# Kernel optimization log

Hardware: AMD Instinct MI355X
Metric: run time of the kernel (lower is better)

The kernel has to match this reference:

```python
import jax, jax.numpy as jnp
import numpy as np

N_ITERS = 200   # fixed PDHG iterations (stands in for SCS max_iters)
POWER_ITERS = 30


def setup_inputs() -> dict:
    key = jax.random.key(0)
    k1, k2 = jax.random.split(key)
    B, n_hos, n_types, n_structs = 512, 16, 16, 4096
    m = n_hos * n_types
    # bids (capacities) are strictly positive counts
    X = jax.random.uniform(k1, (B, n_hos, n_types), jnp.float32, minval=1.0, maxval=10.0)
    # sparse 0/1 cycle-incidence matrix (each column = one feasible exchange structure)
    S = (jax.random.uniform(k2, (m, n_structs)) < 0.03).astype(jnp.float32)
    return {"X": X, "S": S, "batch_size": B}


def _solve_lp_batch(S, b, n_iters=N_ITERS):
    """Batched LP:  max 1^T x  s.t.  x >= 0,  S x <= b,  via Chambolle-Pock PDHG.

    S: [m, n] shared constraint matrix; b: [B, m] per-sample rhs.
    Returns x: [B, n] (the allocation that CvxpyLayer/SCS would return).
    """
    m, n = S.shape
    B = b.shape[0]
    w = jnp.ones((B, n), b.dtype)

    # spectral norm of S via power iteration -> step sizes
    v = jnp.ones((n,), S.dtype)

    def pw(v, _):
        v = S.T @ (S @ v)
        return v / jnp.linalg.norm(v), None

    v, _ = jax.lax.scan(pw, v, None, length=POWER_ITERS)
    L = jnp.sqrt(jnp.vdot(v, S.T @ (S @ v)))  # ~ ||S||_2
    tau = 0.9 / L
    sigma = 0.9 / L

    x0 = jnp.zeros((B, n), b.dtype)
    y0 = jnp.zeros((B, m), b.dtype)  # dual for Sx <= b

    def step(carry, _):
        x, y = carry
        # primal: gradient ascent on w^T x - y^T S x, projected to x >= 0
        x_new = jnp.maximum(x + tau * (w - y @ S), 0.0)        # [B,n]
        # dual: ascent on constraint residual with extrapolated primal, y >= 0
        y_new = jnp.maximum(y + sigma * ((2.0 * x_new - x) @ S.T - b), 0.0)  # [B,m]
        return (x_new, y_new), None

    (x, _), _ = jax.lax.scan(step, (x0, y0), None, length=n_iters)
    return x


def reference(X, S, batch_size):
    m, _ = S.shape
    b = X.reshape(batch_size, m)  # B = X.view(batch, n_hos*n_types)
    return _solve_lp_batch(S, b)  # [batch, n_structures]
```

## Files before the change

kernel.cpp:

```cpp
#include <hip/hip_runtime.h>

#define M 256
#define N 4096
#define NIT 200
#define PIT 30

#define YDUMMY (256*8)
#define ZDUMMY (4096*8)

__global__ void k_colcnt(const float* __restrict__ S, int* __restrict__ col_cnt){
  int j = blockIdx.x*256 + threadIdx.x;
  int c = 0;
  for (int i = 0; i < M; ++i) c += (S[i*N + j] != 0.0f) ? 1 : 0;
  col_cnt[j] = c;
}

__global__ void k_rowcnt(const float* __restrict__ S, int* __restrict__ row_cnt){
  int wid = blockIdx.x*(blockDim.x>>6) + (threadIdx.x>>6);
  int l = threadIdx.x & 63;
  if (wid >= M) return;
  int cnt = 0;
  for (int jc = 0; jc < N/64; ++jc){
    float v = S[wid*N + jc*64 + l];
    unsigned long long mask = __ballot(v != 0.0f);
    cnt += __popcll(mask);
  }
  if (l == 0) row_cnt[wid] = cnt;
}

__global__ void k_sortcol(const int* __restrict__ col_cnt,
                          int* __restrict__ col_perm, int* __restrict__ col_rank){
  __shared__ int cs[N];
  int t0 = threadIdx.x;
  for (int t = 0; t < N/256; ++t) cs[t0 + 256*t] = col_cnt[t0 + 256*t];
  __syncthreads();
  int j = blockIdx.x*256 + t0;
  int cj = cs[j];
  int rank = 0;
  #pragma unroll 4
  for (int jj = 0; jj < N; ++jj){
    int c = cs[jj];
    rank += ((c < cj) || (c == cj && jj < j)) ? 1 : 0;
  }
  col_perm[rank] = j;
  col_rank[j] = rank;
}

__global__ void k_sortrow(const int* __restrict__ row_cnt,
                          int* __restrict__ row_perm, int* __restrict__ row_rank){
  int i = threadIdx.x;
  int ci = row_cnt[i];
  int rank = 0;
  for (int ii = 0; ii < M; ++ii){
    int c = row_cnt[ii];
    rank += ((c < ci) || (c == ci && ii < i)) ? 1 : 0;
  }
  row_perm[rank] = i;
  row_rank[i] = rank;
}

__global__ void k_trips(const int* __restrict__ col_cnt, const int* __restrict__ col_perm,
                        const int* __restrict__ row_cnt, const int* __restrict__ row_perm,
                        int* __restrict__ pT4, int* __restrict__ pB4,
                        int* __restrict__ dT4, int* __restrict__ dB4){
  int tid = threadIdx.x;
  if (tid < 64){
    int k = tid >> 4, w = tid & 15;
    int mx = 0;
    for (int l = 0; l < 64; ++l){
      int s = 64*w + l + 1024*k;
      int c = col_cnt[col_perm[s]];
      mx = max(mx, c);
    }
    pT4[tid] = min((mx + 3) >> 2, 16);
  } else if (tid < 80){
    int w = tid - 64;
    int mx = 0;
    for (int l = 0; l < 64; ++l){
      int t = w*64 + l;
      int r = t >> 2, q = t & 3;
      int len = row_cnt[row_perm[r]];
      int qs = (len*q) >> 2, qe = (len*(q+1)) >> 2;
      mx = max(mx, qe - qs);
    }
    dT4[w] = min((mx + 3) >> 2, 80);
  }
  __syncthreads();
  if (tid == 0){
    int acc = 0;
    for (int i = 0; i < 64; ++i){ pB4[i] = acc; acc += pT4[i]; }
    acc = 0;
    for (int i = 0; i < 16; ++i){ dB4[i] = acc; acc += dT4[i]; }
  }
}

__global__ void k_fillp(const float* __restrict__ S, const int* __restrict__ col_rank,
                        const int* __restrict__ pT4, const int* __restrict__ pB4,
                        unsigned short* __restrict__ pstream){
  int j = blockIdx.x*256 + threadIdx.x;
  int sr = col_rank[j];
  int k = sr >> 10, rem = sr & 1023, w = rem >> 6, l = rem & 63;
  int kw = k*16 + w;
  int base = pB4[kw];
  int cap = pT4[kw]*4;
  int T = l & 15;
  int t = 0;
  for (int cc = 0; cc < 16 && t < cap; ++cc){
    int c = (T + cc) & 15;
    for (int i16 = 0; i16 < 16 && t < cap; ++i16){
      int i = i16*16 + c;
      if (S[i*N + j] != 0.0f){
        pstream[((base + (t>>2))*64 + l)*4 + (t&3)] = (unsigned short)(i*8);
        ++t;
      }
    }
  }
  for (; t < cap; ++t)
    pstream[((base + (t>>2))*64 + l)*4 + (t&3)] = (unsigned short)YDUMMY;
}

__global__ void k_filld(const float* __restrict__ S,
                        const int* __restrict__ row_cnt, const int* __restrict__ row_perm,
                        const int* __restrict__ dT4, const int* __restrict__ dB4,
                        unsigned short* __restrict__ dstream){
  int rr = blockIdx.x;
  int lf = threadIdx.x;
  int i  = row_perm[rr];
  int len = row_cnt[i];
  int c0 = rr & 15;
  int wc = rr >> 4;
  int base = dB4[wc];
  int cap  = dT4[wc]*4;
  int qs1 = (len*1) >> 2, qs2 = (len*2) >> 2, qs3 = (len*3) >> 2;
  int lc0 = (rr & 15) << 2;

  int pos = 0;
  for (int cc = 0; cc < 16; ++cc){
    int c = (c0 + cc) & 15;
    for (int mc = 0; mc < 4; ++mc){
      int m = mc*64 + lf;
      int j = c + 16*m;
      float v = S[i*N + j];
      unsigned long long mask = __ballot(v != 0.0f);
      if (v != 0.0f){
        int rank = pos + __popcll(mask & ((1ull << lf) - 1ull));
        int q = (rank >= qs1) + (rank >= qs2) + (rank >= qs3);
        int qs = (q==0) ? 0 : ((q==1) ? qs1 : ((q==2) ? qs2 : qs3));
        int t = rank - qs;
        if (t < cap)
          dstream[((base + (t>>2))*64 + (lc0 + q))*4 + (t&3)] = (unsigned short)(j*8);
      }
      pos += __popcll(mask);
    }
  }
  if (lf < 4){
    int q = lf;
    int qs = (q==0) ? 0 : ((q==1) ? qs1 : ((q==2) ? qs2 : qs3));
    int qe = (q==3) ? len : ((q==0) ? qs1 : ((q==1) ? qs2 : qs3));
    int qlen = qe - qs; if (qlen > cap) qlen = cap;
    for (int t = qlen; t < cap; ++t)
      dstream[((base + (t>>2))*64 + (lc0 + q))*4 + (t&3)] = (unsigned short)ZDUMMY;
  }
}

__global__ __launch_bounds__(1024) void k_power(
    const ushort4* __restrict__ pstream, const ushort4* __restrict__ dstream,
    const int* __restrict__ col_perm, const int* __restrict__ row_perm,
    const int* __restrict__ pT4, const int* __restrict__ pB4,
    const int* __restrict__ dT4, const int* __restrict__ dB4,
    float* __restrict__ tauw)
{
  __shared__ float2 v_s[N+8];
  __shared__ float2 u_s[M+8];
  __shared__ float2 red2[1024];
  const int tid = threadIdx.x, w = tid >> 6, l = tid & 63;

  int cj[4], pb[4], pt[4];
  float tl[4];
  #pragma unroll
  for (int k = 0; k < 4; ++k){
    int kw = k*16 + w;
    pb[k] = pB4[kw]; pt[k] = pT4[kw];
    cj[k] = col_perm[tid + 1024*k];
    v_s[cj[k]] = make_float2(1.0f, 0.0f);
    tl[k] = 0.0f;
  }
  const int r = tid >> 2, q = tid & 3;
  const int rid = row_perm[r];
  const int db = dB4[w], dt = dT4[w];
  if (tid < 8){ v_s[N+tid] = make_float2(0,0); u_s[M+tid] = make_float2(0,0); }
  __syncthreads();

  const char* vb = (const char*)v_s;
  const char* ub = (const char*)u_s;

  for (int it = 0; it < PIT; ++it){
    float a = 0.0f;
    for (int c = 0; c < dt; ++c){
      ushort4 ix = dstream[(db + c)*64 + l];
      a += ((const float2*)(vb + ix.x))->x + ((const float2*)(vb + ix.y))->x
         + ((const float2*)(vb + ix.z))->x + ((const float2*)(vb + ix.w))->x;
    }
    a += __shfl_xor(a, 1);
    a += __shfl_xor(a, 2);
    if (q == 0) u_s[rid] = make_float2(a, 0.0f);
    __syncthreads();
    #pragma unroll
    for (int k = 0; k < 4; ++k){
      float a2 = 0.0f;
      for (int c = 0; c < pt[k]; ++c){
        ushort4 ix = pstream[(pb[k] + c)*64 + l];
        a2 += ((const float2*)(ub + ix.x))->x + ((const float2*)(ub + ix.y))->x
            + ((const float2*)(ub + ix.z))->x + ((const float2*)(ub + ix.w))->x;
      }
      tl[k] = a2 * (1.0f/1024.0f);
      v_s[cj[k]] = make_float2(tl[k], 0.0f);
    }
    __syncthreads();
  }

  float pv = 0.0f;
  #pragma unroll
  for (int k = 0; k < 4; ++k) pv += tl[k]*tl[k];
  float a = 0.0f;
  for (int c = 0; c < dt; ++c){
    ushort4 ix = dstream[(db + c)*64 + l];
    a += ((const float2*)(vb + ix.x))->x + ((const float2*)(vb + ix.y))->x
       + ((const float2*)(vb + ix.z))->x + ((const float2*)(vb + ix.w))->x;
  }
  a += __shfl_xor(a, 1);
  a += __shfl_xor(a, 2);
  float fsq = (q == 0) ? a*a : 0.0f;
  red2[tid] = make_float2(pv, fsq);
  __syncthreads();
  for (int sd = 512; sd > 0; sd >>= 1){
    if (tid < sd){
      red2[tid].x += red2[tid+sd].x;
      red2[tid].y += red2[tid+sd].y;
    }
    __syncthreads();
  }
  if (tid == 0) tauw[0] = 0.9f * sqrtf(red2[0].x / red2[0].y);
}

__global__ __launch_bounds__(1024) void k_main(
    const float* __restrict__ X,
    const ushort4* __restrict__ pstream, const ushort4* __restrict__ dstream,
    const int* __restrict__ col_perm, const int* __restrict__ row_perm,
    const int* __restrict__ pT4, const int* __restrict__ pB4,
    const int* __restrict__ dT4, const int* __restrict__ dB4,
    const float* __restrict__ tauw, float* __restrict__ out)
{
  __shared__ float2 z_s[N+8];
  __shared__ float2 y_s[M+8];
  const int tid = threadIdx.x, w = tid >> 6, l = tid & 63;
  const int b0 = blockIdx.x * 2;
  const float tau = tauw[0];
  const float sigma = tau;

  int cj[4], pb[4], pt[4];
  float2 x[4];
  #pragma unroll
  for (int k = 0; k < 4; ++k){
    int kw = k*16 + w;
    pb[k] = pB4[kw]; pt[k] = pT4[kw];
    cj[k] = col_perm[tid + 1024*k];
    x[k] = make_float2(0.0f, 0.0f);
  }
  const int r = tid >> 2, q = tid & 3;
  const int rid = row_perm[r];
  const int db = dB4[w], dt = dT4[w];
  float2 bi = make_float2(0,0), yv = make_float2(0,0);
  if (q == 0){
    bi.x = X[b0*M + rid];
    bi.y = X[(b0+1)*M + rid];
    y_s[rid] = make_float2(0,0);
  }
  if (tid < 8){ y_s[M+tid] = make_float2(0,0); z_s[N+tid] = make_float2(0,0); }
  __syncthreads();

  const char* yb = (const char*)y_s;
  const char* zb = (const char*)z_s;

  for (int it = 0; it < NIT; ++it){
    const bool last = (it == NIT-1);
    #pragma unroll
    for (int k = 0; k < 4; ++k){
      float ax = 0.0f, ay = 0.0f;
      for (int c = 0; c < pt[k]; ++c){
        ushort4 ix = pstream[(pb[k] + c)*64 + l];
        float2 a0 = *(const float2*)(yb + ix.x);
        float2 a1 = *(const float2*)(yb + ix.y);
        float2 a2 = *(const float2*)(yb + ix.z);
        float2 a3 = *(const float2*)(yb + ix.w);
        ax += (a0.x + a1.x) + (a2.x + a3.x);
        ay += (a0.y + a1.y) + (a2.y + a3.y);
      }
      float2 xo = x[k];
      float xnx = fmaxf(xo.x + tau*(1.0f - ax), 0.0f);
      float xny = fmaxf(xo.y + tau*(1.0f - ay), 0.0f);
      if (!last) z_s[cj[k]] = make_float2(2.0f*xnx - xo.x, 2.0f*xny - xo.y);
      x[k] = make_float2(xnx, xny);
    }
    if (last) break;
    __syncthreads();
    float ax = 0.0f, ay = 0.0f;
    for (int c = 0; c < dt; ++c){
      ushort4 ix = dstream[(db + c)*64 + l];
      float2 a0 = *(const float2*)(zb + ix.x);
      float2 a1 = *(const float2*)(zb + ix.y);
      float2 a2 = *(const float2*)(zb + ix.z);
      float2 a3 = *(const float2*)(zb + ix.w);
      ax += (a0.x + a1.x) + (a2.x + a3.x);
      ay += (a0.y + a1.y) + (a2.y + a3.y);
    }
    ax += __shfl_xor(ax, 1);  ay += __shfl_xor(ay, 1);
    ax += __shfl_xor(ax, 2);  ay += __shfl_xor(ay, 2);
    if (q == 0){
      yv.x = fmaxf(yv.x + sigma*(ax - bi.x), 0.0f);
      yv.y = fmaxf(yv.y + sigma*(ay - bi.y), 0.0f);
      y_s[rid] = yv;
    }
    __syncthreads();
  }

  #pragma unroll
  for (int k = 0; k < 4; ++k){
    out[(size_t)b0*N + cj[k]]     = x[k].x;
    out[(size_t)(b0+1)*N + cj[k]] = x[k].y;
  }
}

extern "C" void kernel_launch(void* const* d_in, const int* in_sizes, int n_in,
                              void* d_out, int out_size, void* d_ws, size_t ws_size,
                              hipStream_t stream)
{
  const float* X = (const float*)d_in[0];
  const float* S = (const float*)d_in[1];
  float* out = (float*)d_out;
  const int B = in_sizes[0] / M;

  char* p = (char*)d_ws;
  auto alloc = [&](size_t bytes)->char*{
    char* q = p; p += (bytes + 255) & ~size_t(255); return q;
  };
  int* col_cnt  = (int*)alloc(N*sizeof(int));
  int* col_perm = (int*)alloc(N*sizeof(int));
  int* col_rank = (int*)alloc(N*sizeof(int));
  int* row_cnt  = (int*)alloc(M*sizeof(int));
  int* row_perm = (int*)alloc(M*sizeof(int));
  int* row_rank = (int*)alloc(M*sizeof(int));
  int* pT4      = (int*)alloc(64*sizeof(int));
  int* pB4      = (int*)alloc(64*sizeof(int));
  int* dT4      = (int*)alloc(16*sizeof(int));
  int* dB4      = (int*)alloc(16*sizeof(int));
  float* tauw   = (float*)alloc(256);
  unsigned short* pstream = (unsigned short*)alloc(65536ull*8);
  unsigned short* dstream = (unsigned short*)alloc(81920ull*8);

  k_colcnt <<<N/256, 256, 0, stream>>>(S, col_cnt);
  k_rowcnt <<<16, 1024, 0, stream>>>(S, row_cnt);
  k_sortcol<<<N/256, 256, 0, stream>>>(col_cnt, col_perm, col_rank);
  k_sortrow<<<1, M, 0, stream>>>(row_cnt, row_perm, row_rank);
  k_trips  <<<1, 256, 0, stream>>>(col_cnt, col_perm, row_cnt, row_perm, pT4, pB4, dT4, dB4);
  k_fillp  <<<N/256, 256, 0, stream>>>(S, col_rank, pT4, pB4, pstream);
  k_filld  <<<M, 64, 0, stream>>>(S, row_cnt, row_perm, dT4, dB4, dstream);
  k_power  <<<1, 1024, 0, stream>>>((const ushort4*)pstream, (const ushort4*)dstream,
                                    col_perm, row_perm, pT4, pB4, dT4, dB4, tauw);
  k_main   <<<B/2, 1024, 0, stream>>>(X, (const ushort4*)pstream, (const ushort4*)dstream,
                                      col_perm, row_perm, pT4, pB4, dT4, dB4, tauw, out);
}
```

Before: 1.301 ms.

## Schedule sparse index streams to spread LDS bank classes across each wave

The preprocessing kernels that build the primal and dual index streams now run one wavefront per stream block. At each step they greedily choose, per lane, which residue-mod-16 class of index to emit next, with wave-wide ballots counting how many lanes already picked each class. The intent is to lower LDS bank conflicts in the main PDHG gather loops, which index shared-memory vectors by these offsets, across all 200 iterations. The cost is much more serial setup work: a full row scan of 4096 entries per lane in k_filld and very small launches (64 and 16 blocks).

```diff
diff --git a/kernel.cpp b/kernel.cpp
--- a/kernel.cpp
+++ b/kernel.cpp
@@ -94,72 +94,156 @@
   }
 }
 
-__global__ void k_fillp(const float* __restrict__ S, const int* __restrict__ col_rank,
-                        const int* __restrict__ pT4, const int* __restrict__ pB4,
-                        unsigned short* __restrict__ pstream){
-  int j = blockIdx.x*256 + threadIdx.x;
-  int sr = col_rank[j];
-  int k = sr >> 10, rem = sr & 1023, w = rem >> 6, l = rem & 63;
-  int kw = k*16 + w;
-  int base = pB4[kw];
-  int cap = pT4[kw]*4;
-  int T = l & 15;
-  int t = 0;
-  for (int cc = 0; cc < 16 && t < cap; ++cc){
-    int c = (T + cc) & 15;
-    for (int i16 = 0; i16 < 16 && t < cap; ++i16){
-      int i = i16*16 + c;
-      if (S[i*N + j] != 0.0f){
-        pstream[((base + (t>>2))*64 + l)*4 + (t&3)] = (unsigned short)(i*8);
-        ++t;
-      }
-    }
-  }
-  for (; t < cap; ++t)
-    pstream[((base + (t>>2))*64 + l)*4 + (t&3)] = (unsigned short)YDUMMY;
-}
-
-__global__ void k_filld(const float* __restrict__ S,
-                        const int* __restrict__ row_cnt, const int* __restrict__ row_perm,
-                        const int* __restrict__ dT4, const int* __restrict__ dB4,
-                        unsigned short* __restrict__ dstream){
-  int rr = blockIdx.x;
-  int lf = threadIdx.x;
-  int i  = row_perm[rr];
-  int len = row_cnt[i];
-  int c0 = rr & 15;
-  int wc = rr >> 4;
-  int base = dB4[wc];
-  int cap  = dT4[wc]*4;
-  int qs1 = (len*1) >> 2, qs2 = (len*2) >> 2, qs3 = (len*3) >> 2;
-  int lc0 = (rr & 15) << 2;
-
-  int pos = 0;
-  for (int cc = 0; cc < 16; ++cc){
-    int c = (c0 + cc) & 15;
-    for (int mc = 0; mc < 4; ++mc){
-      int m = mc*64 + lf;
-      int j = c + 16*m;
-      float v = S[i*N + j];
-      unsigned long long mask = __ballot(v != 0.0f);
-      if (v != 0.0f){
-        int rank = pos + __popcll(mask & ((1ull << lf) - 1ull));
-        int q = (rank >= qs1) + (rank >= qs2) + (rank >= qs3);
-        int qs = (q==0) ? 0 : ((q==1) ? qs1 : ((q==2) ? qs2 : qs3));
-        int t = rank - qs;
-        if (t < cap)
-          dstream[((base + (t>>2))*64 + (lc0 + q))*4 + (t&3)] = (unsigned short)(j*8);
-      }
-      pos += __popcll(mask);
-    }
-  }
-  if (lf < 4){
-    int q = lf;
-    int qs = (q==0) ? 0 : ((q==1) ? qs1 : ((q==2) ? qs2 : qs3));
-    int qe = (q==3) ? len : ((q==0) ? qs1 : ((q==1) ? qs2 : qs3));
-    int qlen = qe - qs; if (qlen > cap) qlen = cap;
-    for (int t = qlen; t < cap; ++t)
-      dstream[((base + (t>>2))*64 + (lc0 + q))*4 + (t&3)] = (unsigned short)ZDUMMY;
+
+__global__ __launch_bounds__(64) void k_fillp(
+    const float* __restrict__ S, const int* __restrict__ col_perm,
+    const int* __restrict__ pT4, const int* __restrict__ pB4,
+    unsigned short* __restrict__ pstream)
+{
+  const int b = blockIdx.x;
+  const int l = threadIdx.x;
+  const int base = pB4[b], cap = pT4[b]*4;
+  const int j = col_perm[64*(b & 15) + l + 1024*(b >> 4)];
+
+  __shared__ unsigned short msk[64][16];
+  unsigned long long remA = 0, remB = 0;
+  int remT = 0;
+  #pragma unroll
+  for (int c = 0; c < 16; ++c) msk[l][c] = 0;
+  for (int i = 0; i < M; ++i){
+    if (S[(size_t)i*N + j] != 0.0f && remT < cap){
+      int c = i & 15, m = i >> 4;
+      msk[l][c] |= (unsigned short)(1u << m);
+      if (c < 8) remA += 1ull << (c*8); else remB += 1ull << ((c-8)*8);
+      ++remT;
+    }
+  }
+
+  unsigned long long cntA = 0, cntB = 0;
+  for (int t = 0; t < cap; ++t){
+    int myround = ((l >> 4) + t) & 3;
+    int pick = 16;
+    for (int r = 0; r < 4; ++r){
+      if (r == myround && remT > 0){
+        bool forced = (remT >= cap - t);
+        int bestc = -1, bestkey = 1 << 30, bestcnt = 0;
+        #pragma unroll
+        for (int c = 0; c < 16; ++c){
+          int rc = (int)(((c < 8) ? (remA >> (c*8)) : (remB >> ((c-8)*8))) & 0xff);
+          if (rc){
+            int cc = (int)(((c < 8) ? (cntA >> (c*8)) : (cntB >> ((c-8)*8))) & 0xff);
+            int key = (cc << 4) | ((c - l) & 15);
+            if (key < bestkey){ bestkey = key; bestc = c; bestcnt = cc; }
+          }
+        }
+        if (bestc >= 0 && (forced || bestcnt < 4)) pick = bestc;
+      }
+      int np = (r == myround) ? pick : 16;
+      #pragma unroll
+      for (int c = 0; c < 16; ++c){
+        int add = (int)__popcll(__ballot(np == c));
+        if (add){
+          if (c < 8) cntA += (unsigned long long)add << (c*8);
+          else       cntB += (unsigned long long)add << ((c-8)*8);
+        }
+      }
+    }
+    unsigned short off;
+    if (pick < 16){
+      unsigned short mm = msk[l][pick];
+      int m = __builtin_ctz((unsigned)mm);
+      msk[l][pick] = (unsigned short)(mm & (mm - 1));
+      if (pick < 8) remA -= 1ull << (pick*8); else remB -= 1ull << ((pick-8)*8);
+      --remT;
+      off = (unsigned short)((pick + 16*m) * 8);
+    } else {
+      off = (unsigned short)YDUMMY;
+    }
+    pstream[((base + (t>>2))*64 + l)*4 + (t&3)] = off;
+  }
+}
+
+__global__ __launch_bounds__(64) void k_filld(
+    const float* __restrict__ S,
+    const int* __restrict__ row_cnt, const int* __restrict__ row_perm,
+    const int* __restrict__ dT4, const int* __restrict__ dB4,
+    unsigned short* __restrict__ dstream)
+{
+  const int w = blockIdx.x;
+  const int l = threadIdx.x;
+  const int base = dB4[w], cap = dT4[w]*4;
+  const int rr = w*16 + (l >> 2);
+  const int q  = l & 3;
+  const int i  = row_perm[rr];
+  const int len = row_cnt[i];
+  const int qs = (len*q) >> 2, qe = (len*(q+1)) >> 2;
+
+  __shared__ unsigned long long msk[64][16][4];
+  unsigned long long remA = 0, remB = 0;
+  int remT = 0;
+  #pragma unroll
+  for (int c = 0; c < 16; ++c)
+    for (int wd = 0; wd < 4; ++wd) msk[l][c][wd] = 0ull;
+
+  int rho = 0;
+  for (int j = 0; j < N; ++j){
+    if (S[(size_t)i*N + j] != 0.0f){
+      if (rho >= qs && rho < qe && remT < cap){
+        int c = j & 15, m = j >> 4;
+        msk[l][c][m >> 6] |= 1ull << (m & 63);
+        if (c < 8) remA += 1ull << (c*8); else remB += 1ull << ((c-8)*8);
+        ++remT;
+      }
+      ++rho;
+    }
+  }
+
+  unsigned long long cntA = 0, cntB = 0;
+  for (int t = 0; t < cap; ++t){
+    int myround = ((l >> 4) + t) & 3;
+    int pick = 16;
+    for (int r = 0; r < 4; ++r){
+      if (r == myround && remT > 0){
+        bool forced = (remT >= cap - t);
+        int bestc = -1, bestkey = 1 << 30, bestcnt = 0;
+        #pragma unroll
+        for (int c = 0; c < 16; ++c){
+          int rc = (int)(((c < 8) ? (remA >> (c*8)) : (remB >> ((c-8)*8))) & 0xff);
+          if (rc){
+            int cc = (int)(((c < 8) ? (cntA >> (c*8)) : (cntB >> ((c-8)*8))) & 0xff);
+            int key = (cc << 4) | ((c - l) & 15);
+            if (key < bestkey){ bestkey = key; bestc = c; bestcnt = cc; }
+          }
+        }
+        if (bestc >= 0 && (forced || bestcnt < 4)) pick = bestc;
+      }
+      int np = (r == myround) ? pick : 16;
+      #pragma unroll
+      for (int c = 0; c < 16; ++c){
+        int add = (int)__popcll(__ballot(np == c));
+        if (add){
+          if (c < 8) cntA += (unsigned long long)add << (c*8);
+          else       cntB += (unsigned long long)add << ((c-8)*8);
+        }
+      }
+    }
+    unsigned short off;
+    if (pick < 16){
+      int wd = 0;
+      unsigned long long mm = msk[l][pick][0];
+      if (!mm){ mm = msk[l][pick][1]; wd = 1; }
+      if (!mm){ mm = msk[l][pick][2]; wd = 2; }
+      if (!mm){ mm = msk[l][pick][3]; wd = 3; }
+      int bit = __builtin_ctzll(mm);
+      msk[l][pick][wd] = mm & (mm - 1);
+      if (pick < 8) remA -= 1ull << (pick*8); else remB -= 1ull << ((pick-8)*8);
+      --remT;
+      int j = pick + 16*(wd*64 + bit);
+      off = (unsigned short)(j * 8);
+    } else {
+      off = (unsigned short)ZDUMMY;
+    }
+    dstream[((base + (t>>2))*64 + l)*4 + (t&3)] = off;
   }
 }
 
@@ -363,8 +447,8 @@
   k_sortcol<<<N/256, 256, 0, stream>>>(col_cnt, col_perm, col_rank);
   k_sortrow<<<1, M, 0, stream>>>(row_cnt, row_perm, row_rank);
   k_trips  <<<1, 256, 0, stream>>>(col_cnt, col_perm, row_cnt, row_perm, pT4, pB4, dT4, dB4);
-  k_fillp  <<<N/256, 256, 0, stream>>>(S, col_rank, pT4, pB4, pstream);
-  k_filld  <<<M, 64, 0, stream>>>(S, row_cnt, row_perm, dT4, dB4, dstream);
+  k_fillp  <<<64, 64, 0, stream>>>(S, col_perm, pT4, pB4, pstream);
+  k_filld  <<<16, 64, 0, stream>>>(S, row_cnt, row_perm, dT4, dB4, dstream);
   k_power  <<<1, 1024, 0, stream>>>((const ushort4*)pstream, (const ushort4*)dstream,
                                     col_perm, row_perm, pT4, pB4, dT4, dB4, tauw);
   k_main   <<<B/2, 1024, 0, stream>>>(X, (const ushort4*)pstream, (const ushort4*)dstream,
```

New measurement: 2.369 ms. 1.82x slower.

## Build bank-conflict-aware sparse index streams with greedy per-slot column scheduling

Applied to the files above, without the earlier changes.

Replaces the simple sorted fill of the primal and dual index streams with a greedy scheduler. For each stream slot it assigns entries so that lanes within a 16-lane group hit distinct residue classes mod 16, which is meant to avoid LDS bank conflicts in the gathers of the main PDHG kernel. The trip counts now also account for the per-class entry counts. The preprocessing becomes serial per quarter-wave (4 threads doing nested greedy loops, and the dual builder scans whole 4096-wide rows per thread), so setup cost rises in exchange for faster main iterations. Streams may also become longer.

```diff
diff --git a/kernel.cpp b/kernel.cpp
--- a/kernel.cpp
+++ b/kernel.cpp
@@ -59,107 +59,267 @@
   row_rank[i] = rank;
 }
 
-__global__ void k_trips(const int* __restrict__ col_cnt, const int* __restrict__ col_perm,
-                        const int* __restrict__ row_cnt, const int* __restrict__ row_perm,
-                        int* __restrict__ pT4, int* __restrict__ pB4,
-                        int* __restrict__ dT4, int* __restrict__ dB4){
-  int tid = threadIdx.x;
-  if (tid < 64){
-    int k = tid >> 4, w = tid & 15;
-    int mx = 0;
-    for (int l = 0; l < 64; ++l){
-      int s = 64*w + l + 1024*k;
-      int c = col_cnt[col_perm[s]];
-      mx = max(mx, c);
-    }
-    pT4[tid] = min((mx + 3) >> 2, 16);
-  } else if (tid < 80){
-    int w = tid - 64;
-    int mx = 0;
-    for (int l = 0; l < 64; ++l){
-      int t = w*64 + l;
-      int r = t >> 2, q = t & 3;
-      int len = row_cnt[row_perm[r]];
-      int qs = (len*q) >> 2, qe = (len*(q+1)) >> 2;
-      mx = max(mx, qe - qs);
-    }
-    dT4[w] = min((mx + 3) >> 2, 80);
-  }
-  __syncthreads();
-  if (tid == 0){
-    int acc = 0;
-    for (int i = 0; i < 64; ++i){ pB4[i] = acc; acc += pT4[i]; }
-    acc = 0;
-    for (int i = 0; i < 16; ++i){ dB4[i] = acc; acc += dT4[i]; }
-  }
-}
-
-__global__ void k_fillp(const float* __restrict__ S, const int* __restrict__ col_rank,
-                        const int* __restrict__ pT4, const int* __restrict__ pB4,
-                        unsigned short* __restrict__ pstream){
-  int j = blockIdx.x*256 + threadIdx.x;
-  int sr = col_rank[j];
-  int k = sr >> 10, rem = sr & 1023, w = rem >> 6, l = rem & 63;
-  int kw = k*16 + w;
-  int base = pB4[kw];
-  int cap = pT4[kw]*4;
-  int T = l & 15;
-  int t = 0;
-  for (int cc = 0; cc < 16 && t < cap; ++cc){
-    int c = (T + cc) & 15;
-    for (int i16 = 0; i16 < 16 && t < cap; ++i16){
-      int i = i16*16 + c;
-      if (S[i*N + j] != 0.0f){
-        pstream[((base + (t>>2))*64 + l)*4 + (t&3)] = (unsigned short)(i*8);
-        ++t;
-      }
-    }
-  }
-  for (; t < cap; ++t)
+__global__ __launch_bounds__(64) void k_tripp(
+    const float* __restrict__ S, const int* __restrict__ col_perm,
+    int* __restrict__ pT4)
+{
+  const int b = blockIdx.x, l = threadIdx.x;
+  const int j = col_perm[64*(b & 15) + l + 1024*(b >> 4)];
+  __shared__ unsigned short msk[64][16];
+  __shared__ int Dq[64];
+  __shared__ int dl[64];
+  #pragma unroll
+  for (int c = 0; c < 16; ++c) msk[l][c] = 0;
+  int cnt = 0;
+  for (int i = 0; i < M; ++i){
+    if (S[(size_t)i*N + j] != 0.0f){ msk[l][i & 15] |= (unsigned short)(1u << (i >> 4)); ++cnt; }
+  }
+  dl[l] = cnt;
+  __syncthreads();
+  { int qr = l >> 4, c = l & 15, s = 0;
+    for (int u = 0; u < 16; ++u) s += __popc((unsigned)msk[qr*16 + u][c]);
+    Dq[l] = s; }
+  __syncthreads();
+  if (l == 0){
+    int T = 0;
+    for (int u = 0; u < 64; ++u){ T = max(T, dl[u]); T = max(T, Dq[u]); }
+    pT4[b] = min((T + 3) >> 2, 16);
+  }
+}
+
+__global__ __launch_bounds__(64) void k_tripd(
+    const float* __restrict__ S,
+    const int* __restrict__ row_cnt, const int* __restrict__ row_perm,
+    int* __restrict__ dT4)
+{
+  const int w = blockIdx.x, l = threadIdx.x;
+  const int rr = w*16 + (l >> 2), q = l & 3;
+  const int i = row_perm[rr];
+  const int len = row_cnt[i];
+  const int qs = (len*q) >> 2, qe = (len*(q+1)) >> 2;
+  __shared__ int cls[64][16];
+  __shared__ int Dq[64];
+  __shared__ int dl[64];
+  #pragma unroll
+  for (int c = 0; c < 16; ++c) cls[l][c] = 0;
+  int rho = 0;
+  for (int jj = 0; jj < N; ++jj){
+    if (S[(size_t)i*N + jj] != 0.0f){
+      if (rho >= qs && rho < qe) cls[l][jj & 15]++;
+      ++rho;
+    }
+  }
+  dl[l] = qe - qs;
+  __syncthreads();
+  { int qr = l >> 4, c = l & 15, s = 0;
+    for (int u = 0; u < 16; ++u) s += cls[qr*16 + u][c];
+    Dq[l] = s; }
+  __syncthreads();
+  if (l == 0){
+    int T = 0;
+    for (int u = 0; u < 64; ++u){ T = max(T, dl[u]); T = max(T, Dq[u]); }
+    dT4[w] = min((T + 3) >> 2, 80);
+  }
+}
+
+__global__ void k_prefix(const int* __restrict__ pT4, int* __restrict__ pB4,
+                         const int* __restrict__ dT4, int* __restrict__ dB4){
+  int acc = 0;
+  for (int i = 0; i < 64; ++i){ pB4[i] = acc; acc += pT4[i]; }
+  acc = 0;
+  for (int i = 0; i < 16; ++i){ dB4[i] = acc; acc += dT4[i]; }
+}
+
+__global__ __launch_bounds__(64) void k_fillp(
+    const float* __restrict__ S, const int* __restrict__ col_perm,
+    const int* __restrict__ pT4, const int* __restrict__ pB4,
+    unsigned short* __restrict__ pstream)
+{
+  const int b = blockIdx.x, l = threadIdx.x;
+  const int base = pB4[b];
+  const int T = pT4[b]*4;
+  const int j = col_perm[64*(b & 15) + l + 1024*(b >> 4)];
+
+  __shared__ unsigned short msk[64][16];
+  __shared__ unsigned short ne[64];
+  __shared__ int Dq[64];
+  __shared__ unsigned long long used[64];
+
+  #pragma unroll
+  for (int c = 0; c < 16; ++c) msk[l][c] = 0;
+  for (int i = 0; i < M; ++i)
+    if (S[(size_t)i*N + j] != 0.0f) msk[l][i & 15] |= (unsigned short)(1u << (i >> 4));
+  { unsigned nn = 0;
+    for (int c = 0; c < 16; ++c) if (msk[l][c]) nn |= 1u << c;
+    ne[l] = (unsigned short)nn; }
+  used[l] = 0ull;
+  for (int t = 0; t < T; ++t)
     pstream[((base + (t>>2))*64 + l)*4 + (t&3)] = (unsigned short)YDUMMY;
-}
-
-__global__ void k_filld(const float* __restrict__ S,
-                        const int* __restrict__ row_cnt, const int* __restrict__ row_perm,
-                        const int* __restrict__ dT4, const int* __restrict__ dB4,
-                        unsigned short* __restrict__ dstream){
-  int rr = blockIdx.x;
-  int lf = threadIdx.x;
-  int i  = row_perm[rr];
-  int len = row_cnt[i];
-  int c0 = rr & 15;
-  int wc = rr >> 4;
-  int base = dB4[wc];
-  int cap  = dT4[wc]*4;
-  int qs1 = (len*1) >> 2, qs2 = (len*2) >> 2, qs3 = (len*3) >> 2;
-  int lc0 = (rr & 15) << 2;
-
-  int pos = 0;
-  for (int cc = 0; cc < 16; ++cc){
-    int c = (c0 + cc) & 15;
-    for (int mc = 0; mc < 4; ++mc){
-      int m = mc*64 + lf;
-      int j = c + 16*m;
-      float v = S[i*N + j];
-      unsigned long long mask = __ballot(v != 0.0f);
-      if (v != 0.0f){
-        int rank = pos + __popcll(mask & ((1ull << lf) - 1ull));
-        int q = (rank >= qs1) + (rank >= qs2) + (rank >= qs3);
-        int qs = (q==0) ? 0 : ((q==1) ? qs1 : ((q==2) ? qs2 : qs3));
-        int t = rank - qs;
-        if (t < cap)
-          dstream[((base + (t>>2))*64 + (lc0 + q))*4 + (t&3)] = (unsigned short)(j*8);
-      }
-      pos += __popcll(mask);
-    }
-  }
-  if (lf < 4){
-    int q = lf;
-    int qs = (q==0) ? 0 : ((q==1) ? qs1 : ((q==2) ? qs2 : qs3));
-    int qe = (q==3) ? len : ((q==0) ? qs1 : ((q==1) ? qs2 : qs3));
-    int qlen = qe - qs; if (qlen > cap) qlen = cap;
-    for (int t = qlen; t < cap; ++t)
-      dstream[((base + (t>>2))*64 + (lc0 + q))*4 + (t&3)] = (unsigned short)ZDUMMY;
+  __syncthreads();
+  { int qr = l >> 4, c = l & 15, s = 0;
+    for (int u = 0; u < 16; ++u) s += __popc((unsigned)msk[qr*16 + u][c]);
+    Dq[l] = s; }
+  __syncthreads();
+
+  if (l < 4){
+    const int qr = l;
+    for (int t = 0; t < T; ++t){
+      unsigned freec = 0xFFFFu, am = 0;
+      for (int pass = 0; pass < 16; ++pass){
+        int bu = -1, bpc = 99; unsigned bav = 0;
+        for (int u = 0; u < 16; ++u){
+          if (am & (1u << u)) continue;
+          unsigned av = (unsigned)ne[qr*16 + u] & freec;
+          if (!av) continue;
+          int pc = __popc(av);
+          if (pc < bpc){ bpc = pc; bu = u; bav = av; }
+        }
+        if (bu < 0) break;
+        int bc = -1, bd = -1;
+        for (int c = 0; c < 16; ++c)
+          if ((bav >> c) & 1){ int d = Dq[qr*16 + c]; if (d > bd){ bd = d; bc = c; } }
+        int lane = qr*16 + bu;
+        unsigned mm = (unsigned)msk[lane][bc];
+        int m = __ffs(mm) - 1;
+        mm &= mm - 1;
+        msk[lane][bc] = (unsigned short)mm;
+        if (!mm) ne[lane] = (unsigned short)(ne[lane] & ~(1u << bc));
+        Dq[qr*16 + bc]--;
+        freec &= ~(1u << bc);
+        am |= 1u << bu;
+        used[lane] |= 1ull << t;
+        pstream[((base + (t>>2))*64 + lane)*4 + (t&3)] = (unsigned short)(((bc + 16*m))*8);
+      }
+    }
+    unsigned long long tmask = (T >= 64) ? ~0ull : ((1ull << T) - 1ull);
+    for (int u = 0; u < 16; ++u){
+      int lane = qr*16 + u;
+      while (ne[lane]){
+        int c = __ffs((unsigned)ne[lane]) - 1;
+        unsigned mm = (unsigned)msk[lane][c];
+        int m = __ffs(mm) - 1;
+        mm &= mm - 1;
+        msk[lane][c] = (unsigned short)mm;
+        if (!mm) ne[lane] = (unsigned short)(ne[lane] & ~(1u << c));
+        unsigned long long fr = ~used[lane] & tmask;
+        if (!fr) break;
+        int t = __ffsll(fr) - 1;
+        used[lane] |= 1ull << t;
+        pstream[((base + (t>>2))*64 + lane)*4 + (t&3)] = (unsigned short)(((c + 16*m))*8);
+      }
+    }
+  }
+}
+
+__global__ __launch_bounds__(64) void k_filld(
+    const float* __restrict__ S,
+    const int* __restrict__ row_cnt, const int* __restrict__ row_perm,
+    const int* __restrict__ dT4, const int* __restrict__ dB4,
+    unsigned short* __restrict__ dstream)
+{
+  const int w = blockIdx.x, l = threadIdx.x;
+  const int base = dB4[w];
+  const int T = dT4[w]*4;
+  const int rr = w*16 + (l >> 2), q = l & 3;
+  const int i = row_perm[rr];
+  const int len = row_cnt[i];
+  const int qs = (len*q) >> 2, qe = (len*(q+1)) >> 2;
+
+  __shared__ unsigned long long msk[64][16][4];
+  __shared__ unsigned short ne[64];
+  __shared__ int Dq[64];
+  __shared__ unsigned long long used[64][5];
+
+  #pragma unroll
+  for (int c = 0; c < 16; ++c)
+    for (int wd = 0; wd < 4; ++wd) msk[l][c][wd] = 0ull;
+  int rho = 0;
+  for (int jj = 0; jj < N; ++jj){
+    if (S[(size_t)i*N + jj] != 0.0f){
+      if (rho >= qs && rho < qe){
+        int m = jj >> 4;
+        msk[l][jj & 15][m >> 6] |= 1ull << (m & 63);
+      }
+      ++rho;
+    }
+  }
+  { unsigned nn = 0;
+    for (int c = 0; c < 16; ++c)
+      if (msk[l][c][0] | msk[l][c][1] | msk[l][c][2] | msk[l][c][3]) nn |= 1u << c;
+    ne[l] = (unsigned short)nn; }
+  for (int wd = 0; wd < 5; ++wd) used[l][wd] = 0ull;
+  for (int t = 0; t < T; ++t)
+    dstream[((base + (t>>2))*64 + l)*4 + (t&3)] = (unsigned short)ZDUMMY;
+  __syncthreads();
+  { int qr = l >> 4, c = l & 15, s = 0;
+    for (int u = 0; u < 16; ++u){
+      s += (int)__popcll(msk[qr*16+u][c][0]) + (int)__popcll(msk[qr*16+u][c][1])
+         + (int)__popcll(msk[qr*16+u][c][2]) + (int)__popcll(msk[qr*16+u][c][3]);
+    }
+    Dq[l] = s; }
+  __syncthreads();
+
+  if (l < 4){
+    const int qr = l;
+    for (int t = 0; t < T; ++t){
+      unsigned freec = 0xFFFFu, am = 0;
+      for (int pass = 0; pass < 16; ++pass){
+        int bu = -1, bpc = 99; unsigned bav = 0;
+        for (int u = 0; u < 16; ++u){
+          if (am & (1u << u)) continue;
+          unsigned av = (unsigned)ne[qr*16 + u] & freec;
+          if (!av) continue;
+          int pc = __popc(av);
+          if (pc < bpc){ bpc = pc; bu = u; bav = av; }
+        }
+        if (bu < 0) break;
+        int bc = -1, bd = -1;
+        for (int c = 0; c < 16; ++c)
+          if ((bav >> c) & 1){ int d = Dq[qr*16 + c]; if (d > bd){ bd = d; bc = c; } }
+        int lane = qr*16 + bu;
+        int wd = 0;
+        unsigned long long mm = msk[lane][bc][0];
+        if (!mm){ mm = msk[lane][bc][1]; wd = 1; }
+        if (!mm){ mm = msk[lane][bc][2]; wd = 2; }
+        if (!mm){ mm = msk[lane][bc][3]; wd = 3; }
+        int bit = __ffsll(mm) - 1;
+        msk[lane][bc][wd] = mm & (mm - 1);
+        if (!(msk[lane][bc][0] | msk[lane][bc][1] | msk[lane][bc][2] | msk[lane][bc][3]))
+          ne[lane] = (unsigned short)(ne[lane] & ~(1u << bc));
+        Dq[qr*16 + bc]--;
+        freec &= ~(1u << bc);
+        am |= 1u << bu;
+        used[lane][t >> 6] |= 1ull << (t & 63);
+        int jj = bc + 16*(wd*64 + bit);
+        dstream[((base + (t>>2))*64 + lane)*4 + (t&3)] = (unsigned short)(jj*8);
+      }
+    }
+    for (int u = 0; u < 16; ++u){
+      int lane = qr*16 + u;
+      while (ne[lane]){
+        int c = __ffs((unsigned)ne[lane]) - 1;
+        int wd = 0;
+        unsigned long long mm = msk[lane][c][0];
+        if (!mm){ mm = msk[lane][c][1]; wd = 1; }
+        if (!mm){ mm = msk[lane][c][2]; wd = 2; }
+        if (!mm){ mm = msk[lane][c][3]; wd = 3; }
+        int bit = __ffsll(mm) - 1;
+        msk[lane][c][wd] = mm & (mm - 1);
+        if (!(msk[lane][c][0] | msk[lane][c][1] | msk[lane][c][2] | msk[lane][c][3]))
+          ne[lane] = (unsigned short)(ne[lane] & ~(1u << c));
+        int t = -1;
+        for (int w5 = 0; w5 < 5 && t < 0; ++w5){
+          int width = T - 64*w5; if (width <= 0) break;
+          unsigned long long wm = (width >= 64) ? ~0ull : ((1ull << width) - 1ull);
+          unsigned long long fr = ~used[lane][w5] & wm;
+          if (fr) t = 64*w5 + (__ffsll(fr) - 1);
+        }
+        if (t < 0) break;
+        used[lane][t >> 6] |= 1ull << (t & 63);
+        int jj = c + 16*(wd*64 + bit);
+        dstream[((base + (t>>2))*64 + lane)*4 + (t&3)] = (unsigned short)(jj*8);
+      }
+    }
   }
 }
 
@@ -362,9 +522,11 @@
   k_rowcnt <<<16, 1024, 0, stream>>>(S, row_cnt);
   k_sortcol<<<N/256, 256, 0, stream>>>(col_cnt, col_perm, col_rank);
   k_sortrow<<<1, M, 0, stream>>>(row_cnt, row_perm, row_rank);
-  k_trips  <<<1, 256, 0, stream>>>(col_cnt, col_perm, row_cnt, row_perm, pT4, pB4, dT4, dB4);
-  k_fillp  <<<N/256, 256, 0, stream>>>(S, col_rank, pT4, pB4, pstream);
-  k_filld  <<<M, 64, 0, stream>>>(S, row_cnt, row_perm, dT4, dB4, dstream);
+  k_tripp  <<<64, 64, 0, stream>>>(S, col_perm, pT4);
+  k_tripd  <<<16, 64, 0, stream>>>(S, row_cnt, row_perm, dT4);
+  k_prefix <<<1, 1, 0, stream>>>(pT4, pB4, dT4, dB4);
+  k_fillp  <<<64, 64, 0, stream>>>(S, col_perm, pT4, pB4, pstream);
+  k_filld  <<<16, 64, 0, stream>>>(S, row_cnt, row_perm, dT4, dB4, dstream);
   k_power  <<<1, 1024, 0, stream>>>((const ushort4*)pstream, (const ushort4*)dstream,
                                     col_perm, row_perm, pT4, pB4, dT4, dB4, tauw);
   k_main   <<<B/2, 1024, 0, stream>>>(X, (const ushort4*)pstream, (const ushort4*)dstream,
```

Result: slower. 4.154 ms (+219.3%).

## Compute spectral norm via dense Gram matrix from row bitmasks instead of sparse power iteration

Applied to the files above, without the earlier changes.

Row nonzero bitmasks are stored during row counting and used to build the 256x256 Gram matrix S S^T with popcounts. Power iteration then runs on this dense matrix held in shared memory, replacing the gather-based sparse S^T S iteration over 4096 columns in a single block. The starting vector and scaling differ slightly, so the tau estimate could shift a little. The fill kernels also drop their rotated column and row traversal order and use a simple linear scan.

```diff
diff --git a/kernel.cpp b/kernel.cpp
--- a/kernel.cpp
+++ b/kernel.cpp
@@ -15,7 +15,9 @@
   col_cnt[j] = c;
 }
 
-__global__ void k_rowcnt(const float* __restrict__ S, int* __restrict__ row_cnt){
+__global__ void k_rowmask(const float* __restrict__ S,
+                          unsigned long long* __restrict__ rowmaskT,
+                          int* __restrict__ row_cnt){
   int wid = blockIdx.x*(blockDim.x>>6) + (threadIdx.x>>6);
   int l = threadIdx.x & 63;
   if (wid >= M) return;
@@ -23,6 +25,7 @@
   for (int jc = 0; jc < N/64; ++jc){
     float v = S[wid*N + jc*64 + l];
     unsigned long long mask = __ballot(v != 0.0f);
+    if (l == 0) rowmaskT[jc*M + wid] = mask;
     cnt += __popcll(mask);
   }
   if (l == 0) row_cnt[wid] = cnt;
@@ -98,21 +101,16 @@
                         const int* __restrict__ pT4, const int* __restrict__ pB4,
                         unsigned short* __restrict__ pstream){
   int j = blockIdx.x*256 + threadIdx.x;
-  int sr = col_rank[j];
-  int k = sr >> 10, rem = sr & 1023, w = rem >> 6, l = rem & 63;
+  int s = col_rank[j];
+  int k = s >> 10, rem = s & 1023, w = rem >> 6, l = rem & 63;
   int kw = k*16 + w;
   int base = pB4[kw];
   int cap = pT4[kw]*4;
-  int T = l & 15;
   int t = 0;
-  for (int cc = 0; cc < 16 && t < cap; ++cc){
-    int c = (T + cc) & 15;
-    for (int i16 = 0; i16 < 16 && t < cap; ++i16){
-      int i = i16*16 + c;
-      if (S[i*N + j] != 0.0f){
-        pstream[((base + (t>>2))*64 + l)*4 + (t&3)] = (unsigned short)(i*8);
-        ++t;
-      }
+  for (int i = 0; i < M && t < cap; ++i){
+    if (S[i*N + j] != 0.0f){
+      pstream[((base + (t>>2))*64 + l)*4 + (t&3)] = (unsigned short)(i*8);
+      ++t;
     }
   }
   for (; t < cap; ++t)
@@ -127,31 +125,26 @@
   int lf = threadIdx.x;
   int i  = row_perm[rr];
   int len = row_cnt[i];
-  int c0 = rr & 15;
-  int wc = rr >> 4;
-  int base = dB4[wc];
-  int cap  = dT4[wc]*4;
+  int w = rr >> 4;
+  int base = dB4[w];
+  int cap  = dT4[w]*4;
   int qs1 = (len*1) >> 2, qs2 = (len*2) >> 2, qs3 = (len*3) >> 2;
   int lc0 = (rr & 15) << 2;
 
   int pos = 0;
-  for (int cc = 0; cc < 16; ++cc){
-    int c = (c0 + cc) & 15;
-    for (int mc = 0; mc < 4; ++mc){
-      int m = mc*64 + lf;
-      int j = c + 16*m;
-      float v = S[i*N + j];
-      unsigned long long mask = __ballot(v != 0.0f);
-      if (v != 0.0f){
-        int rank = pos + __popcll(mask & ((1ull << lf) - 1ull));
-        int q = (rank >= qs1) + (rank >= qs2) + (rank >= qs3);
-        int qs = (q==0) ? 0 : ((q==1) ? qs1 : ((q==2) ? qs2 : qs3));
-        int t = rank - qs;
-        if (t < cap)
-          dstream[((base + (t>>2))*64 + (lc0 + q))*4 + (t&3)] = (unsigned short)(j*8);
-      }
-      pos += __popcll(mask);
-    }
+  for (int jc = 0; jc < N/64; ++jc){
+    int j = jc*64 + lf;
+    float v = S[i*N + j];
+    unsigned long long mask = __ballot(v != 0.0f);
+    if (v != 0.0f){
+      int rank = pos + __popcll(mask & ((1ull << lf) - 1ull));
+      int q = (rank >= qs1) + (rank >= qs2) + (rank >= qs3);
+      int qs = (q==0) ? 0 : ((q==1) ? qs1 : ((q==2) ? qs2 : qs3));
+      int t = rank - qs;
+      if (t < cap)
+        dstream[((base + (t>>2))*64 + (lc0 + q))*4 + (t&3)] = (unsigned short)(j*8);
+    }
+    pos += __popcll(mask);
   }
   if (lf < 4){
     int q = lf;
@@ -163,84 +156,74 @@
   }
 }
 
-__global__ __launch_bounds__(1024) void k_power(
-    const ushort4* __restrict__ pstream, const ushort4* __restrict__ dstream,
-    const int* __restrict__ col_perm, const int* __restrict__ row_perm,
-    const int* __restrict__ pT4, const int* __restrict__ pB4,
-    const int* __restrict__ dT4, const int* __restrict__ dB4,
+__global__ __launch_bounds__(256) void k_gram(
+    const unsigned long long* __restrict__ rowmaskT,
+    unsigned short* __restrict__ G)
+{
+  __shared__ unsigned long long mi[64];
+  const int i = blockIdx.x, t = threadIdx.x;
+  if (t < 64) mi[t] = rowmaskT[t*M + i];
+  __syncthreads();
+  int acc = 0;
+  #pragma unroll 8
+  for (int w = 0; w < 64; ++w)
+    acc += (int)__popcll(mi[w] & rowmaskT[w*M + t]);
+  G[i*M + t] = (unsigned short)acc;
+}
+
+__global__ __launch_bounds__(1024) void k_powerG(
+    const unsigned short* __restrict__ G, const int* __restrict__ row_cnt,
     float* __restrict__ tauw)
 {
-  __shared__ float2 v_s[N+8];
-  __shared__ float2 u_s[M+8];
-  __shared__ float2 red2[1024];
-  const int tid = threadIdx.x, w = tid >> 6, l = tid & 63;
-
-  int cj[4], pb[4], pt[4];
-  float tl[4];
-  #pragma unroll
-  for (int k = 0; k < 4; ++k){
-    int kw = k*16 + w;
-    pb[k] = pB4[kw]; pt[k] = pT4[kw];
-    cj[k] = col_perm[tid + 1024*k];
-    v_s[cj[k]] = make_float2(1.0f, 0.0f);
-    tl[k] = 0.0f;
-  }
-  const int r = tid >> 2, q = tid & 3;
-  const int rid = row_perm[r];
-  const int db = dB4[w], dt = dT4[w];
-  if (tid < 8){ v_s[N+tid] = make_float2(0,0); u_s[M+tid] = make_float2(0,0); }
-  __syncthreads();
-
-  const char* vb = (const char*)v_s;
-  const char* ub = (const char*)u_s;
+  __shared__ unsigned short Gs[M*M];
+  __shared__ float uA[M], uB[M];
+  __shared__ float part[1024];
+  const int t = threadIdx.x;
+  const int r = t & 255, q = t >> 8;
+
+  {
+    const unsigned* g32 = (const unsigned*)G;
+    unsigned* s32 = (unsigned*)Gs;
+    for (int k = 0; k < (M*M/2)/1024; ++k) s32[t + 1024*k] = g32[t + 1024*k];
+  }
+  if (t < M){ uA[t] = (float)row_cnt[t]; }
+  __syncthreads();
 
   for (int it = 0; it < PIT; ++it){
-    float a = 0.0f;
-    for (int c = 0; c < dt; ++c){
-      ushort4 ix = dstream[(db + c)*64 + l];
-      a += ((const float2*)(vb + ix.x))->x + ((const float2*)(vb + ix.y))->x
-         + ((const float2*)(vb + ix.z))->x + ((const float2*)(vb + ix.w))->x;
-    }
-    a += __shfl_xor(a, 1);
-    a += __shfl_xor(a, 2);
-    if (q == 0) u_s[rid] = make_float2(a, 0.0f);
-    __syncthreads();
-    #pragma unroll
-    for (int k = 0; k < 4; ++k){
-      float a2 = 0.0f;
-      for (int c = 0; c < pt[k]; ++c){
-        ushort4 ix = pstream[(pb[k] + c)*64 + l];
-        a2 += ((const float2*)(ub + ix.x))->x + ((const float2*)(ub + ix.y))->x
-            + ((const float2*)(ub + ix.z))->x + ((const float2*)(ub + ix.w))->x;
-      }
-      tl[k] = a2 * (1.0f/1024.0f);
-      v_s[cj[k]] = make_float2(tl[k], 0.0f);
-    }
-    __syncthreads();
-  }
-
-  float pv = 0.0f;
-  #pragma unroll
-  for (int k = 0; k < 4; ++k) pv += tl[k]*tl[k];
-  float a = 0.0f;
-  for (int c = 0; c < dt; ++c){
-    ushort4 ix = dstream[(db + c)*64 + l];
-    a += ((const float2*)(vb + ix.x))->x + ((const float2*)(vb + ix.y))->x
-       + ((const float2*)(vb + ix.z))->x + ((const float2*)(vb + ix.w))->x;
-  }
-  a += __shfl_xor(a, 1);
-  a += __shfl_xor(a, 2);
-  float fsq = (q == 0) ? a*a : 0.0f;
-  red2[tid] = make_float2(pv, fsq);
+    const float* src = (it & 1) ? uB : uA;
+    float* dst = (it & 1) ? uA : uB;
+    float acc = 0.0f;
+    #pragma unroll 8
+    for (int c = 0; c < 64; ++c){
+      int cc = q*64 + c;
+      acc += (float)Gs[cc*M + r] * src[cc];
+    }
+    part[t] = acc;
+    __syncthreads();
+    if (t < M)
+      dst[r] = (part[r] + part[r+256] + part[r+512] + part[r+768]) * (1.0f/1024.0f);
+    __syncthreads();
+  }
+  float cc_ = 0.0f, ac_ = 0.0f;
+  if (t < M){ cc_ = uA[t]*uA[t]; ac_ = uB[t]*uA[t]; }
+  part[t] = cc_;
   __syncthreads();
   for (int sd = 512; sd > 0; sd >>= 1){
-    if (tid < sd){
-      red2[tid].x += red2[tid+sd].x;
-      red2[tid].y += red2[tid+sd].y;
-    }
-    __syncthreads();
-  }
-  if (tid == 0) tauw[0] = 0.9f * sqrtf(red2[0].x / red2[0].y);
+    if (t < sd) part[t] += part[t+sd];
+    __syncthreads();
+  }
+  float ccs = part[0];
+  __syncthreads();
+  part[t] = ac_;
+  __syncthreads();
+  for (int sd = 512; sd > 0; sd >>= 1){
+    if (t < sd) part[t] += part[t+sd];
+    __syncthreads();
+  }
+  if (t == 0){
+    float acs = part[0];
+    tauw[0] = 0.9f * sqrtf(acs / ccs) * (1.0f/32.0f);
+  }
 }
 
 __global__ __launch_bounds__(1024) void k_main(
@@ -355,18 +338,20 @@
   int* dT4      = (int*)alloc(16*sizeof(int));
   int* dB4      = (int*)alloc(16*sizeof(int));
   float* tauw   = (float*)alloc(256);
+  unsigned long long* rowmaskT = (unsigned long long*)alloc((N/64)*M*sizeof(unsigned long long));
+  unsigned short* G       = (unsigned short*)alloc((size_t)M*M*sizeof(unsigned short));
   unsigned short* pstream = (unsigned short*)alloc(65536ull*8);
   unsigned short* dstream = (unsigned short*)alloc(81920ull*8);
 
   k_colcnt <<<N/256, 256, 0, stream>>>(S, col_cnt);
-  k_rowcnt <<<16, 1024, 0, stream>>>(S, row_cnt);
+  k_rowmask<<<16, 1024, 0, stream>>>(S, rowmaskT, row_cnt);
   k_sortcol<<<N/256, 256, 0, stream>>>(col_cnt, col_perm, col_rank);
   k_sortrow<<<1, M, 0, stream>>>(row_cnt, row_perm, row_rank);
   k_trips  <<<1, 256, 0, stream>>>(col_cnt, col_perm, row_cnt, row_perm, pT4, pB4, dT4, dB4);
   k_fillp  <<<N/256, 256, 0, stream>>>(S, col_rank, pT4, pB4, pstream);
   k_filld  <<<M, 64, 0, stream>>>(S, row_cnt, row_perm, dT4, dB4, dstream);
-  k_power  <<<1, 1024, 0, stream>>>((const ushort4*)pstream, (const ushort4*)dstream,
-                                    col_perm, row_perm, pT4, pB4, dT4, dB4, tauw);
+  k_gram   <<<M, 256, 0, stream>>>(rowmaskT, G);
+  k_powerG <<<1, 1024, 0, stream>>>(G, row_cnt, tauw);
   k_main   <<<B/2, 1024, 0, stream>>>(X, (const ushort4*)pstream, (const ushort4*)dstream,
                                       col_perm, row_perm, pT4, pB4, dT4, dB4, tauw, out);
 }
```

Measured after the change: 1.231 ms. 1.06x faster.
